# Kernel tuning notes

Hardware: AMD Instinct MI355X
Metric: run time of the kernel (lower is better)

The kernel has to match this reference:

```python
import jax, jax.numpy as jnp
import numpy as np

N, H, C = 65536, 256, 512  # tokens, hidden_dim, cond_dim


def setup_inputs() -> dict:
    key = jax.random.key(0)
    ks = jax.random.split(key, 8)
    s_h = 1.0 / np.sqrt(H)
    s_c = 1.0 / np.sqrt(C)
    return {
        "x": jax.random.normal(ks[0], (N, H), dtype=jnp.float32),
        "cond": jax.random.normal(ks[1], (N, C), dtype=jnp.float32),
        # FiLM: Linear(cond_dim -> 2*hidden_dim), output split into (gamma, beta)
        "W_film": jax.random.uniform(ks[2], (C, 2 * H), jnp.float32, -s_c, s_c),
        "b_film": jax.random.uniform(ks[3], (2 * H,), jnp.float32, -s_c, s_c),
        "W1": jax.random.uniform(ks[4], (H, H), jnp.float32, -s_h, s_h),
        "b1": jax.random.uniform(ks[5], (H,), jnp.float32, -s_h, s_h),
        "W2": jax.random.uniform(ks[6], (H, H), jnp.float32, -s_h, s_h),
        "b2": jax.random.uniform(ks[7], (H,), jnp.float32, -s_h, s_h),
    }


def reference(x, cond, W_film, b_film, W1, b1, W2, b2):
    # FiLM conditioning: gamma * x + beta (cond path; LayerNorm branch unused)
    gb = cond @ W_film + b_film            # [N, 2H]
    gamma, beta = gb[:, :H], gb[:, H:]
    h = gamma * x + beta
    # Dropout is identity in eval mode.
    h = jax.nn.relu(h) @ W1 + b1           # [N, H]
    h = jax.nn.relu(h) @ W2 + b2           # [N, H]
    return h + x                            # residual
```

## Files before the change

### kernel.cpp

```cpp
#include <hip/hip_runtime.h>
#include <hip/hip_bf16.h>


typedef __attribute__((ext_vector_type(8))) short bf16x8;
typedef __attribute__((ext_vector_type(4))) float f32x4;

typedef unsigned short ushort_t;
typedef unsigned int uint_t;

__device__ __forceinline__ ushort_t f2bfh(float f) {
  __hip_bfloat16 h = __float2bfloat16(f);
  return *reinterpret_cast<ushort_t*>(&h);
}
__device__ __forceinline__ float bf2f(ushort_t s) {
  union { uint_t u; float f; } v; v.u = ((uint_t)s) << 16;
  return v.f;
}
__device__ __forceinline__ bf16x8 ldfrag(const ushort_t* p) {
  return *reinterpret_cast<const bf16x8*>(p);
}
__device__ __forceinline__ bf16x8 pack8(float4 a, float4 b) {
  union { bf16x8 v; __hip_bfloat162 h[4]; } u;
  u.h[0] = __float22bfloat162_rn(float2{a.x, a.y});
  u.h[1] = __float22bfloat162_rn(float2{a.z, a.w});
  u.h[2] = __float22bfloat162_rn(float2{b.x, b.y});
  u.h[3] = __float22bfloat162_rn(float2{b.z, b.w});
  return u.v;
}

__global__ void pack_weights(const float* __restrict__ Wf,
                             const float* __restrict__ W1,
                             const float* __restrict__ W2,
                             ushort_t* __restrict__ p1,
                             ushort_t* __restrict__ pW1,
                             ushort_t* __restrict__ pW2) {
  int u = blockIdx.x * 256 + threadIdx.x;
  if (u < 32768) {
    int lane = u & 63, rest = u >> 6;
    int kt = rest & 15;
    int kb = kt * 32 + (lane >> 4) * 8;
    int col = (rest >> 4) * 16 + (lane & 15);
#pragma unroll
    for (int j = 0; j < 8; ++j)
      p1[(size_t)u * 8 + j] = f2bfh(Wf[(size_t)(kb + j) * 512 + col]);
  } else if (u < 40960) {
    int v = u - 32768;
    int lane = v & 63;
    int kt = (v >> 6) & 7;
    int kb = kt * 32 + (lane >> 4) * 8;
    int col = (v >> 9) * 16 + (lane & 15);
#pragma unroll
    for (int j = 0; j < 8; ++j)
      pW1[(size_t)v * 8 + j] = f2bfh(W1[(size_t)(kb + j) * 256 + col]);
  } else if (u < 49152) {
    int v = u - 40960;
    int lane = v & 63;
    int kt = (v >> 6) & 7;
    int kb = kt * 32 + (lane >> 4) * 8;
    int col = (v >> 9) * 16 + (lane & 15);
#pragma unroll
    for (int j = 0; j < 8; ++j)
      pW2[(size_t)v * 8 + j] = f2bfh(W2[(size_t)(kb + j) * 256 + col]);
  }
}

__global__ __launch_bounds__(512, 2)
void film_fused(const float* __restrict__ x, const float* __restrict__ cond,
                const float* __restrict__ b_film, const float* __restrict__ b1,
                const float* __restrict__ b2,
                const ushort_t* __restrict__ p1, const ushort_t* __restrict__ pW1,
                const ushort_t* __restrict__ pW2, float* __restrict__ out) {
  __shared__ __align__(16) char lds[65536];
  const int r0 = blockIdx.x * 64;
  const int t = threadIdx.x;
  const int w = t >> 6;
  const int l = t & 63;
  const int l15 = l & 15;
  const int lhi = l >> 4;

  float bfv[4], b1v[2], b2v[2];
#pragma unroll
  for (int tt = 0; tt < 4; ++tt) bfv[tt] = b_film[w * 64 + tt * 16 + l15];
#pragma unroll
  for (int tt = 0; tt < 2; ++tt) {
    int col = w * 32 + tt * 16 + l15;
    b1v[tt] = b1[col];
    b2v[tt] = b2[col];
  }

#pragma unroll
  for (int it = 0; it < 8; ++it) {
    int u = it * 512 + t;
    int row = u >> 6, k8 = u & 63;
    const float4* cs = reinterpret_cast<const float4*>(cond + (size_t)(r0 + row) * 512 + k8 * 8);
    float4 a = cs[0], b = cs[1];
    int byte = row * 1024 + k8 * 16;
    byte ^= ((row & 15) << 4);
    *reinterpret_cast<bf16x8*>(lds + byte) = pack8(a, b);
  }
  bf16x8 bb[2][4];
#pragma unroll
  for (int tt = 0; tt < 4; ++tt)
    bb[0][tt] = ldfrag(p1 + ((size_t)((w * 4 + tt) * 16 + 0) * 64 + l) * 8);
  __syncthreads();

  f32x4 acc[4][4];
#pragma unroll
  for (int m = 0; m < 4; ++m)
#pragma unroll
    for (int n = 0; n < 4; ++n) acc[m][n] = (f32x4){0.f, 0.f, 0.f, 0.f};

#pragma unroll
  for (int kt = 0; kt < 16; ++kt) {
    const int cur = kt & 1;
    if (kt < 15) {
#pragma unroll
      for (int tt = 0; tt < 4; ++tt)
        bb[cur ^ 1][tt] = ldfrag(p1 + ((size_t)((w * 4 + tt) * 16 + kt + 1) * 64 + l) * 8);
    }
    bf16x8 afr[4];
#pragma unroll
    for (int m = 0; m < 4; ++m) {
      int row = m * 16 + l15;
      int byte = row * 1024 + kt * 64 + lhi * 16;
      byte ^= ((row & 15) << 4);
      afr[m] = *reinterpret_cast<const bf16x8*>(lds + byte);
    }
    __builtin_amdgcn_s_setprio(1);
#pragma unroll
    for (int tt = 0; tt < 4; ++tt)
#pragma unroll
      for (int m = 0; m < 4; ++m)
        acc[m][tt] = __builtin_amdgcn_mfma_f32_16x16x32_bf16(afr[m], bb[cur][tt], acc[m][tt], 0, 0, 0);
    __builtin_amdgcn_s_setprio(0);
  }
  __syncthreads();

#pragma unroll
  for (int tt = 0; tt < 4; ++tt) {
    int col = w * 64 + tt * 16 + l15;
#pragma unroll
    for (int m = 0; m < 4; ++m) {
#pragma unroll
      for (int reg = 0; reg < 4; ++reg) {
        int row = m * 16 + lhi * 4 + reg;
        int byte = row * 1024 + col * 2;
        byte ^= ((row & 15) << 4);
        *reinterpret_cast<ushort_t*>(lds + byte) = f2bfh(acc[m][tt][reg] + bfv[tt]);
      }
    }
  }
  bf16x8 bb2[2][2];
#pragma unroll
  for (int tt = 0; tt < 2; ++tt)
    bb2[0][tt] = ldfrag(pW1 + ((size_t)((w * 2 + tt) * 8 + 0) * 64 + l) * 8);
  __syncthreads();

#pragma unroll
  for (int i = 0; i < 4; ++i) {
    int u = i * 512 + t;
    int row = u >> 5, c8 = u & 31;
    int gbyte = row * 1024 + c8 * 16;
    gbyte ^= ((row & 15) << 4);
    int bbyte = row * 1024 + 512 + c8 * 16;
    bbyte ^= ((row & 15) << 4);
    union { bf16x8 v; ushort_t s[8]; } g, be, r;
    g.v = *reinterpret_cast<const bf16x8*>(lds + gbyte);
    be.v = *reinterpret_cast<const bf16x8*>(lds + bbyte);
    const float4* xs = reinterpret_cast<const float4*>(x + (size_t)(r0 + row) * 256 + c8 * 8);
    float4 xa = xs[0], xb = xs[1];
    float xv[8] = {xa.x, xa.y, xa.z, xa.w, xb.x, xb.y, xb.z, xb.w};
#pragma unroll
    for (int j = 0; j < 8; ++j)
      r.s[j] = f2bfh(fmaxf(bf2f(g.s[j]) * xv[j] + bf2f(be.s[j]), 0.f));
    *reinterpret_cast<bf16x8*>(lds + gbyte) = r.v;
  }
  __syncthreads();

  f32x4 acc2[4][2];
#pragma unroll
  for (int m = 0; m < 4; ++m)
#pragma unroll
    for (int n = 0; n < 2; ++n) acc2[m][n] = (f32x4){0.f, 0.f, 0.f, 0.f};

#pragma unroll
  for (int kt = 0; kt < 8; ++kt) {
    const int cur = kt & 1;
    if (kt < 7) {
#pragma unroll
      for (int tt = 0; tt < 2; ++tt)
        bb2[cur ^ 1][tt] = ldfrag(pW1 + ((size_t)((w * 2 + tt) * 8 + kt + 1) * 64 + l) * 8);
    }
    bf16x8 afr[4];
#pragma unroll
    for (int m = 0; m < 4; ++m) {
      int row = m * 16 + l15;
      int byte = row * 1024 + kt * 64 + lhi * 16;
      byte ^= ((row & 15) << 4);
      afr[m] = *reinterpret_cast<const bf16x8*>(lds + byte);
    }
    __builtin_amdgcn_s_setprio(1);
#pragma unroll
    for (int tt = 0; tt < 2; ++tt)
#pragma unroll
      for (int m = 0; m < 4; ++m)
        acc2[m][tt] = __builtin_amdgcn_mfma_f32_16x16x32_bf16(afr[m], bb2[cur][tt], acc2[m][tt], 0, 0, 0);
    __builtin_amdgcn_s_setprio(0);
  }

  bf16x8 bb3[2][2];
#pragma unroll
  for (int tt = 0; tt < 2; ++tt)
    bb3[0][tt] = ldfrag(pW2 + ((size_t)((w * 2 + tt) * 8 + 0) * 64 + l) * 8);
#pragma unroll
  for (int tt = 0; tt < 2; ++tt) {
    int col = w * 32 + tt * 16 + l15;
#pragma unroll
    for (int m = 0; m < 4; ++m) {
#pragma unroll
      for (int reg = 0; reg < 4; ++reg) {
        int row = m * 16 + lhi * 4 + reg;
        int byte = row * 1024 + 512 + col * 2;
        byte ^= ((row & 15) << 4);
        *reinterpret_cast<ushort_t*>(lds + byte) = f2bfh(fmaxf(acc2[m][tt][reg] + b1v[tt], 0.f));
      }
    }
  }
  __syncthreads();

  f32x4 acc3[4][2];
#pragma unroll
  for (int m = 0; m < 4; ++m)
#pragma unroll
    for (int n = 0; n < 2; ++n) acc3[m][n] = (f32x4){0.f, 0.f, 0.f, 0.f};

#pragma unroll
  for (int kt = 0; kt < 8; ++kt) {
    const int cur = kt & 1;
    if (kt < 7) {
#pragma unroll
      for (int tt = 0; tt < 2; ++tt)
        bb3[cur ^ 1][tt] = ldfrag(pW2 + ((size_t)((w * 2 + tt) * 8 + kt + 1) * 64 + l) * 8);
    }
    bf16x8 afr[4];
#pragma unroll
    for (int m = 0; m < 4; ++m) {
      int row = m * 16 + l15;
      int byte = row * 1024 + 512 + kt * 64 + lhi * 16;
      byte ^= ((row & 15) << 4);
      afr[m] = *reinterpret_cast<const bf16x8*>(lds + byte);
    }
    __builtin_amdgcn_s_setprio(1);
#pragma unroll
    for (int tt = 0; tt < 2; ++tt)
#pragma unroll
      for (int m = 0; m < 4; ++m)
        acc3[m][tt] = __builtin_amdgcn_mfma_f32_16x16x32_bf16(afr[m], bb3[cur][tt], acc3[m][tt], 0, 0, 0);
    __builtin_amdgcn_s_setprio(0);
  }
  __syncthreads();

#pragma unroll
  for (int hh = 0; hh < 2; ++hh) {
    if (hh) __syncthreads();
#pragma unroll
    for (int tt = 0; tt < 2; ++tt) {
      int col = w * 32 + tt * 16 + l15;
#pragma unroll
      for (int mm = 0; mm < 2; ++mm) {
        int m = hh * 2 + mm;
#pragma unroll
        for (int reg = 0; reg < 4; ++reg) {
          int r = mm * 16 + lhi * 4 + reg;
          int byte = r * 1024 + col * 4;
          byte ^= ((r & 15) << 4);
          *reinterpret_cast<float*>(lds + byte) = acc3[m][tt][reg] + b2v[tt];
        }
      }
    }
    __syncthreads();
#pragma unroll
    for (int i = 0; i < 4; ++i) {
      int u = i * 512 + t;
      int r = u >> 6, c4 = u & 63;
      int byte = r * 1024 + c4 * 16;
      byte ^= ((r & 15) << 4);
      f32x4 v = *reinterpret_cast<const f32x4*>(lds + byte);
      int grow = hh * 32 + r;
      const float4 xres = *reinterpret_cast<const float4*>(
          x + (size_t)(r0 + grow) * 256 + c4 * 4);
      v.x += xres.x; v.y += xres.y; v.z += xres.z; v.w += xres.w;
      f32x4* op = reinterpret_cast<f32x4*>(out + (size_t)(r0 + grow) * 256 + c4 * 4);
      __builtin_nontemporal_store(v, op);
    }
  }
}

extern "C" void kernel_launch(void* const* d_in, const int* in_sizes, int n_in,
                              void* d_out, int out_size, void* d_ws, size_t ws_size,
                              hipStream_t stream) {
  const float* x      = (const float*)d_in[0];
  const float* cond   = (const float*)d_in[1];
  const float* W_film = (const float*)d_in[2];
  const float* b_film = (const float*)d_in[3];
  const float* W1     = (const float*)d_in[4];
  const float* b1     = (const float*)d_in[5];
  const float* W2     = (const float*)d_in[6];
  const float* b2     = (const float*)d_in[7];
  float* out = (float*)d_out;

  ushort_t* p1  = (ushort_t*)d_ws;
  ushort_t* pW1 = p1 + 262144;
  ushort_t* pW2 = pW1 + 65536;

  hipLaunchKernelGGL(pack_weights, dim3(192), dim3(256), 0, stream,
                     W_film, W1, W2, p1, pW1, pW2);
  hipLaunchKernelGGL(film_fused, dim3(1024), dim3(512), 0, stream,
                     x, cond, b_film, b1, b2, p1, pW1, pW2, out);
}
```

Baseline: 99.48 us.

## Stream cond tiles into an LDS ring via async global_load_lds

The upfront cond load now bypasses registers. Each 64-column fp32 chunk is fetched asynchronously with global_load_lds into a four-slot LDS ring and prefetched two chunks ahead of the FiLM GEMM. Fragments are read back as fp32 from the XOR-swizzled slots and packed to bf16 just before the MFMA. The aim is to overlap the cond fetch with matrix work instead of stalling on one large staging phase. The cost is double the LDS read traffic, bf16 conversion inside the MFMA loop, and a barrier every chunk, which may also force full vmcnt waits.

```diff
diff --git a/kernel.cpp b/kernel.cpp
--- a/kernel.cpp
+++ b/kernel.cpp
@@ -25,6 +25,14 @@
   u.h[1] = __float22bfloat162_rn(float2{a.z, a.w});
   u.h[2] = __float22bfloat162_rn(float2{b.x, b.y});
   u.h[3] = __float22bfloat162_rn(float2{b.z, b.w});
+  return u.v;
+}
+__device__ __forceinline__ bf16x8 pack8v(f32x4 a, f32x4 b) {
+  union { bf16x8 v; __hip_bfloat162 h[4]; } u;
+  u.h[0] = __float22bfloat162_rn(float2{a[0], a[1]});
+  u.h[1] = __float22bfloat162_rn(float2{a[2], a[3]});
+  u.h[2] = __float22bfloat162_rn(float2{b[0], b[1]});
+  u.h[3] = __float22bfloat162_rn(float2{b[2], b[3]});
   return u.v;
 }
 
@@ -88,16 +96,24 @@
     b2v[tt] = b2[col];
   }
 
-#pragma unroll
-  for (int it = 0; it < 8; ++it) {
-    int u = it * 512 + t;
-    int row = u >> 6, k8 = u & 63;
-    const float4* cs = reinterpret_cast<const float4*>(cond + (size_t)(r0 + row) * 512 + k8 * 8);
-    float4 a = cs[0], b = cs[1];
-    int byte = row * 1024 + k8 * 16;
-    byte ^= ((row & 15) << 4);
-    *reinterpret_cast<bf16x8*>(lds + byte) = pack8(a, b);
-  }
+  const char* condb = reinterpret_cast<const char*>(cond);
+#define STAGE_CHUNK(c)                                                        \
+  {                                                                           \
+    char* qb = lds + ((c) & 3) * 16384;                                       \
+    _Pragma("unroll")                                                         \
+    for (int i = 0; i < 2; ++i) {                                             \
+      int u = i * 512 + t;                                                    \
+      int row = u >> 4, slot = u & 15;                                        \
+      const char* g = condb + (size_t)(r0 + row) * 2048 + (c) * 256 +         \
+                      ((slot ^ (row & 15)) << 4);                             \
+      __builtin_amdgcn_global_load_lds(                                       \
+          (const __attribute__((address_space(1))) void*)g,                   \
+          (__attribute__((address_space(3))) void*)(qb + u * 16), 16, 0, 0);  \
+    }                                                                         \
+  }
+
+  STAGE_CHUNK(0)
+  STAGE_CHUNK(1)
   bf16x8 bb[2][4];
 #pragma unroll
   for (int tt = 0; tt < 4; ++tt)
@@ -111,30 +127,38 @@
     for (int n = 0; n < 4; ++n) acc[m][n] = (f32x4){0.f, 0.f, 0.f, 0.f};
 
 #pragma unroll
-  for (int kt = 0; kt < 16; ++kt) {
-    const int cur = kt & 1;
-    if (kt < 15) {
+  for (int c = 0; c < 8; ++c) {
+    if (c < 6) STAGE_CHUNK(c + 2)
+    const char* qb = lds + (c & 3) * 16384;
+#pragma unroll
+    for (int ktl = 0; ktl < 2; ++ktl) {
+      const int kt = c * 2 + ktl;
+      const int cur = kt & 1;
+      if (kt < 15) {
+#pragma unroll
+        for (int tt = 0; tt < 4; ++tt)
+          bb[cur ^ 1][tt] = ldfrag(p1 + ((size_t)((w * 4 + tt) * 16 + kt + 1) * 64 + l) * 8);
+      }
+      bf16x8 afr[4];
+#pragma unroll
+      for (int m = 0; m < 4; ++m) {
+        int row = m * 16 + l15;
+        int sw = row & 15;
+        int s0 = ktl * 8 + lhi * 2;
+        f32x4 f0 = *reinterpret_cast<const f32x4*>(qb + row * 256 + ((s0 ^ sw) << 4));
+        f32x4 f1 = *reinterpret_cast<const f32x4*>(qb + row * 256 + (((s0 + 1) ^ sw) << 4));
+        afr[m] = pack8v(f0, f1);
+      }
+      __builtin_amdgcn_s_setprio(1);
 #pragma unroll
       for (int tt = 0; tt < 4; ++tt)
-        bb[cur ^ 1][tt] = ldfrag(p1 + ((size_t)((w * 4 + tt) * 16 + kt + 1) * 64 + l) * 8);
-    }
-    bf16x8 afr[4];
-#pragma unroll
-    for (int m = 0; m < 4; ++m) {
-      int row = m * 16 + l15;
-      int byte = row * 1024 + kt * 64 + lhi * 16;
-      byte ^= ((row & 15) << 4);
-      afr[m] = *reinterpret_cast<const bf16x8*>(lds + byte);
-    }
-    __builtin_amdgcn_s_setprio(1);
-#pragma unroll
-    for (int tt = 0; tt < 4; ++tt)
-#pragma unroll
-      for (int m = 0; m < 4; ++m)
-        acc[m][tt] = __builtin_amdgcn_mfma_f32_16x16x32_bf16(afr[m], bb[cur][tt], acc[m][tt], 0, 0, 0);
-    __builtin_amdgcn_s_setprio(0);
-  }
-  __syncthreads();
+#pragma unroll
+        for (int m = 0; m < 4; ++m)
+          acc[m][tt] = __builtin_amdgcn_mfma_f32_16x16x32_bf16(afr[m], bb[cur][tt], acc[m][tt], 0, 0, 0);
+      __builtin_amdgcn_s_setprio(0);
+    }
+    __syncthreads();
+  }
 
 #pragma unroll
   for (int tt = 0; tt < 4; ++tt) {
@@ -294,6 +318,7 @@
       __builtin_nontemporal_store(v, op);
     }
   }
+#undef STAGE_CHUNK
 }
 
 extern "C" void kernel_launch(void* const* d_in, const int* in_sizes, int n_in,
```

After: 97.54 us. About the same (-1.9%).

## Shrink row tile to 32 with 16 waves per block and fuse FiLM epilogue

Applied to the files above, without the earlier changes.

Each block now handles 32 rows with 1024 threads, so each wave owns one 16-column slice of gamma and beta plus a 16-column slice of the hidden outputs. LDS drops to 32 KB and per-wave accumulators shrink, which raises the launch bound to 4 blocks per CU. The FiLM multiply-add is applied directly from the gamma and beta accumulators against x staged in LDS, so the bf16 gb round trip through LDS is gone. The cost is less register reuse of weight fragments per row and more global weight fragment loads per output row, plus non-unrolled K loops. x is also rounded to bf16 before the FiLM multiply, which adds a small precision loss.

```diff
diff --git a/kernel.cpp b/kernel.cpp
--- a/kernel.cpp
+++ b/kernel.cpp
@@ -64,33 +64,30 @@
   }
 }
 
-__global__ __launch_bounds__(512, 2)
+__global__ __launch_bounds__(1024, 4)
 void film_fused(const float* __restrict__ x, const float* __restrict__ cond,
                 const float* __restrict__ b_film, const float* __restrict__ b1,
                 const float* __restrict__ b2,
                 const ushort_t* __restrict__ p1, const ushort_t* __restrict__ pW1,
                 const ushort_t* __restrict__ pW2, float* __restrict__ out) {
-  __shared__ __align__(16) char lds[65536];
-  const int r0 = blockIdx.x * 64;
+  __shared__ __align__(16) char lds[32768];
+  char* A = lds;
+  char* B = lds + 16384;
+  const int r0 = blockIdx.x * 32;
   const int t = threadIdx.x;
   const int w = t >> 6;
   const int l = t & 63;
   const int l15 = l & 15;
   const int lhi = l >> 4;
 
-  float bfv[4], b1v[2], b2v[2];
-#pragma unroll
-  for (int tt = 0; tt < 4; ++tt) bfv[tt] = b_film[w * 64 + tt * 16 + l15];
-#pragma unroll
-  for (int tt = 0; tt < 2; ++tt) {
-    int col = w * 32 + tt * 16 + l15;
-    b1v[tt] = b1[col];
-    b2v[tt] = b2[col];
-  }
-
-#pragma unroll
-  for (int it = 0; it < 8; ++it) {
-    int u = it * 512 + t;
+  const float bgv = b_film[w * 16 + l15];
+  const float bbv = b_film[256 + w * 16 + l15];
+  const float b1v = b1[w * 16 + l15];
+  const float b2v = b2[w * 16 + l15];
+
+#pragma unroll
+  for (int it = 0; it < 2; ++it) {
+    int u = it * 1024 + t;
     int row = u >> 6, k8 = u & 63;
     const float4* cs = reinterpret_cast<const float4*>(cond + (size_t)(r0 + row) * 512 + k8 * 8);
     float4 a = cs[0], b = cs[1];
@@ -98,201 +95,177 @@
     byte ^= ((row & 15) << 4);
     *reinterpret_cast<bf16x8*>(lds + byte) = pack8(a, b);
   }
-  bf16x8 bb[2][4];
-#pragma unroll
-  for (int tt = 0; tt < 4; ++tt)
-    bb[0][tt] = ldfrag(p1 + ((size_t)((w * 4 + tt) * 16 + 0) * 64 + l) * 8);
-  __syncthreads();
-
-  f32x4 acc[4][4];
-#pragma unroll
-  for (int m = 0; m < 4; ++m)
-#pragma unroll
-    for (int n = 0; n < 4; ++n) acc[m][n] = (f32x4){0.f, 0.f, 0.f, 0.f};
-
-#pragma unroll
-  for (int kt = 0; kt < 16; ++kt) {
-    const int cur = kt & 1;
-    if (kt < 15) {
-#pragma unroll
-      for (int tt = 0; tt < 4; ++tt)
-        bb[cur ^ 1][tt] = ldfrag(p1 + ((size_t)((w * 4 + tt) * 16 + kt + 1) * 64 + l) * 8);
-    }
-    bf16x8 afr[4];
-#pragma unroll
-    for (int m = 0; m < 4; ++m) {
-      int row = m * 16 + l15;
-      int byte = row * 1024 + kt * 64 + lhi * 16;
-      byte ^= ((row & 15) << 4);
-      afr[m] = *reinterpret_cast<const bf16x8*>(lds + byte);
-    }
-    __builtin_amdgcn_s_setprio(1);
-#pragma unroll
-    for (int tt = 0; tt < 4; ++tt)
-#pragma unroll
-      for (int m = 0; m < 4; ++m)
-        acc[m][tt] = __builtin_amdgcn_mfma_f32_16x16x32_bf16(afr[m], bb[cur][tt], acc[m][tt], 0, 0, 0);
-    __builtin_amdgcn_s_setprio(0);
-  }
-  __syncthreads();
-
-#pragma unroll
-  for (int tt = 0; tt < 4; ++tt) {
-    int col = w * 64 + tt * 16 + l15;
-#pragma unroll
-    for (int m = 0; m < 4; ++m) {
-#pragma unroll
-      for (int reg = 0; reg < 4; ++reg) {
-        int row = m * 16 + lhi * 4 + reg;
-        int byte = row * 1024 + col * 2;
-        byte ^= ((row & 15) << 4);
-        *reinterpret_cast<ushort_t*>(lds + byte) = f2bfh(acc[m][tt][reg] + bfv[tt]);
-      }
-    }
-  }
-  bf16x8 bb2[2][2];
-#pragma unroll
-  for (int tt = 0; tt < 2; ++tt)
-    bb2[0][tt] = ldfrag(pW1 + ((size_t)((w * 2 + tt) * 8 + 0) * 64 + l) * 8);
-  __syncthreads();
-
-#pragma unroll
-  for (int i = 0; i < 4; ++i) {
-    int u = i * 512 + t;
-    int row = u >> 5, c8 = u & 31;
-    int gbyte = row * 1024 + c8 * 16;
-    gbyte ^= ((row & 15) << 4);
-    int bbyte = row * 1024 + 512 + c8 * 16;
-    bbyte ^= ((row & 15) << 4);
-    union { bf16x8 v; ushort_t s[8]; } g, be, r;
-    g.v = *reinterpret_cast<const bf16x8*>(lds + gbyte);
-    be.v = *reinterpret_cast<const bf16x8*>(lds + bbyte);
+  bf16x8 bcg = ldfrag(p1 + ((size_t)(w * 16 + 0) * 64 + l) * 8);
+  bf16x8 bcb = ldfrag(p1 + ((size_t)((16 + w) * 16 + 0) * 64 + l) * 8);
+  __syncthreads();
+
+  f32x4 accg[2], accb[2];
+#pragma unroll
+  for (int m = 0; m < 2; ++m) {
+    accg[m] = (f32x4){0.f, 0.f, 0.f, 0.f};
+    accb[m] = (f32x4){0.f, 0.f, 0.f, 0.f};
+  }
+
+#pragma unroll 1
+  for (int kp = 0; kp < 8; ++kp) {
+    const int kt0 = kp * 2;
+    bf16x8 bng = ldfrag(p1 + ((size_t)(w * 16 + kt0 + 1) * 64 + l) * 8);
+    bf16x8 bnb = ldfrag(p1 + ((size_t)((16 + w) * 16 + kt0 + 1) * 64 + l) * 8);
+    __builtin_amdgcn_s_setprio(1);
+#pragma unroll
+    for (int m = 0; m < 2; ++m) {
+      int row = m * 16 + l15;
+      int byte = row * 1024 + kt0 * 64 + lhi * 16;
+      byte ^= ((row & 15) << 4);
+      bf16x8 a = *reinterpret_cast<const bf16x8*>(lds + byte);
+      accg[m] = __builtin_amdgcn_mfma_f32_16x16x32_bf16(a, bcg, accg[m], 0, 0, 0);
+      accb[m] = __builtin_amdgcn_mfma_f32_16x16x32_bf16(a, bcb, accb[m], 0, 0, 0);
+    }
+    __builtin_amdgcn_s_setprio(0);
+    if (kt0 + 2 < 16) {
+      bcg = ldfrag(p1 + ((size_t)(w * 16 + kt0 + 2) * 64 + l) * 8);
+      bcb = ldfrag(p1 + ((size_t)((16 + w) * 16 + kt0 + 2) * 64 + l) * 8);
+    }
+    __builtin_amdgcn_s_setprio(1);
+#pragma unroll
+    for (int m = 0; m < 2; ++m) {
+      int row = m * 16 + l15;
+      int byte = row * 1024 + (kt0 + 1) * 64 + lhi * 16;
+      byte ^= ((row & 15) << 4);
+      bf16x8 a = *reinterpret_cast<const bf16x8*>(lds + byte);
+      accg[m] = __builtin_amdgcn_mfma_f32_16x16x32_bf16(a, bng, accg[m], 0, 0, 0);
+      accb[m] = __builtin_amdgcn_mfma_f32_16x16x32_bf16(a, bnb, accb[m], 0, 0, 0);
+    }
+    __builtin_amdgcn_s_setprio(0);
+  }
+  __syncthreads();
+
+  {
+    int row = t >> 5, c8 = t & 31;
     const float4* xs = reinterpret_cast<const float4*>(x + (size_t)(r0 + row) * 256 + c8 * 8);
     float4 xa = xs[0], xb = xs[1];
-    float xv[8] = {xa.x, xa.y, xa.z, xa.w, xb.x, xb.y, xb.z, xb.w};
-#pragma unroll
-    for (int j = 0; j < 8; ++j)
-      r.s[j] = f2bfh(fmaxf(bf2f(g.s[j]) * xv[j] + bf2f(be.s[j]), 0.f));
-    *reinterpret_cast<bf16x8*>(lds + gbyte) = r.v;
-  }
-  __syncthreads();
-
-  f32x4 acc2[4][2];
-#pragma unroll
-  for (int m = 0; m < 4; ++m)
-#pragma unroll
-    for (int n = 0; n < 2; ++n) acc2[m][n] = (f32x4){0.f, 0.f, 0.f, 0.f};
-
-#pragma unroll
-  for (int kt = 0; kt < 8; ++kt) {
-    const int cur = kt & 1;
-    if (kt < 7) {
-#pragma unroll
-      for (int tt = 0; tt < 2; ++tt)
-        bb2[cur ^ 1][tt] = ldfrag(pW1 + ((size_t)((w * 2 + tt) * 8 + kt + 1) * 64 + l) * 8);
-    }
-    bf16x8 afr[4];
-#pragma unroll
-    for (int m = 0; m < 4; ++m) {
-      int row = m * 16 + l15;
-      int byte = row * 1024 + kt * 64 + lhi * 16;
-      byte ^= ((row & 15) << 4);
-      afr[m] = *reinterpret_cast<const bf16x8*>(lds + byte);
-    }
-    __builtin_amdgcn_s_setprio(1);
-#pragma unroll
-    for (int tt = 0; tt < 2; ++tt)
-#pragma unroll
-      for (int m = 0; m < 4; ++m)
-        acc2[m][tt] = __builtin_amdgcn_mfma_f32_16x16x32_bf16(afr[m], bb2[cur][tt], acc2[m][tt], 0, 0, 0);
-    __builtin_amdgcn_s_setprio(0);
-  }
-
-  bf16x8 bb3[2][2];
-#pragma unroll
-  for (int tt = 0; tt < 2; ++tt)
-    bb3[0][tt] = ldfrag(pW2 + ((size_t)((w * 2 + tt) * 8 + 0) * 64 + l) * 8);
-#pragma unroll
-  for (int tt = 0; tt < 2; ++tt) {
-    int col = w * 32 + tt * 16 + l15;
-#pragma unroll
-    for (int m = 0; m < 4; ++m) {
-#pragma unroll
-      for (int reg = 0; reg < 4; ++reg) {
-        int row = m * 16 + lhi * 4 + reg;
-        int byte = row * 1024 + 512 + col * 2;
-        byte ^= ((row & 15) << 4);
-        *reinterpret_cast<ushort_t*>(lds + byte) = f2bfh(fmaxf(acc2[m][tt][reg] + b1v[tt], 0.f));
-      }
-    }
-  }
-  __syncthreads();
-
-  f32x4 acc3[4][2];
-#pragma unroll
-  for (int m = 0; m < 4; ++m)
-#pragma unroll
-    for (int n = 0; n < 2; ++n) acc3[m][n] = (f32x4){0.f, 0.f, 0.f, 0.f};
-
-#pragma unroll
-  for (int kt = 0; kt < 8; ++kt) {
-    const int cur = kt & 1;
-    if (kt < 7) {
-#pragma unroll
-      for (int tt = 0; tt < 2; ++tt)
-        bb3[cur ^ 1][tt] = ldfrag(pW2 + ((size_t)((w * 2 + tt) * 8 + kt + 1) * 64 + l) * 8);
-    }
-    bf16x8 afr[4];
-#pragma unroll
-    for (int m = 0; m < 4; ++m) {
-      int row = m * 16 + l15;
-      int byte = row * 1024 + 512 + kt * 64 + lhi * 16;
-      byte ^= ((row & 15) << 4);
-      afr[m] = *reinterpret_cast<const bf16x8*>(lds + byte);
-    }
-    __builtin_amdgcn_s_setprio(1);
-#pragma unroll
-    for (int tt = 0; tt < 2; ++tt)
-#pragma unroll
-      for (int m = 0; m < 4; ++m)
-        acc3[m][tt] = __builtin_amdgcn_mfma_f32_16x16x32_bf16(afr[m], bb3[cur][tt], acc3[m][tt], 0, 0, 0);
-    __builtin_amdgcn_s_setprio(0);
-  }
-  __syncthreads();
-
-#pragma unroll
-  for (int hh = 0; hh < 2; ++hh) {
-    if (hh) __syncthreads();
-#pragma unroll
-    for (int tt = 0; tt < 2; ++tt) {
-      int col = w * 32 + tt * 16 + l15;
-#pragma unroll
-      for (int mm = 0; mm < 2; ++mm) {
-        int m = hh * 2 + mm;
-#pragma unroll
-        for (int reg = 0; reg < 4; ++reg) {
-          int r = mm * 16 + lhi * 4 + reg;
-          int byte = r * 1024 + col * 4;
-          byte ^= ((r & 15) << 4);
-          *reinterpret_cast<float*>(lds + byte) = acc3[m][tt][reg] + b2v[tt];
-        }
-      }
-    }
-    __syncthreads();
-#pragma unroll
-    for (int i = 0; i < 4; ++i) {
-      int u = i * 512 + t;
-      int r = u >> 6, c4 = u & 63;
-      int byte = r * 1024 + c4 * 16;
-      byte ^= ((r & 15) << 4);
-      f32x4 v = *reinterpret_cast<const f32x4*>(lds + byte);
-      int grow = hh * 32 + r;
-      const float4 xres = *reinterpret_cast<const float4*>(
-          x + (size_t)(r0 + grow) * 256 + c4 * 4);
-      v.x += xres.x; v.y += xres.y; v.z += xres.z; v.w += xres.w;
-      f32x4* op = reinterpret_cast<f32x4*>(out + (size_t)(r0 + grow) * 256 + c4 * 4);
-      __builtin_nontemporal_store(v, op);
-    }
+    int byte = row * 512 + c8 * 16;
+    byte ^= ((row & 15) << 4);
+    *reinterpret_cast<bf16x8*>(A + byte) = pack8(xa, xb);
+  }
+  __syncthreads();
+
+#pragma unroll
+  for (int m = 0; m < 2; ++m) {
+#pragma unroll
+    for (int reg = 0; reg < 4; ++reg) {
+      int row = m * 16 + lhi * 4 + reg;
+      int col = w * 16 + l15;
+      int byte = row * 512 + col * 2;
+      byte ^= ((row & 15) << 4);
+      float xv = bf2f(*reinterpret_cast<const ushort_t*>(A + byte));
+      float hv = fmaxf((accg[m][reg] + bgv) * xv + (accb[m][reg] + bbv), 0.f);
+      *reinterpret_cast<ushort_t*>(B + byte) = f2bfh(hv);
+    }
+  }
+  bf16x8 c2 = ldfrag(pW1 + ((size_t)(w * 8 + 0) * 64 + l) * 8);
+  __syncthreads();
+
+  f32x4 acc2[2];
+#pragma unroll
+  for (int m = 0; m < 2; ++m) acc2[m] = (f32x4){0.f, 0.f, 0.f, 0.f};
+
+#pragma unroll 1
+  for (int kp = 0; kp < 4; ++kp) {
+    const int kt0 = kp * 2;
+    bf16x8 n2 = ldfrag(pW1 + ((size_t)(w * 8 + kt0 + 1) * 64 + l) * 8);
+    __builtin_amdgcn_s_setprio(1);
+#pragma unroll
+    for (int m = 0; m < 2; ++m) {
+      int row = m * 16 + l15;
+      int byte = row * 512 + kt0 * 64 + lhi * 16;
+      byte ^= ((row & 15) << 4);
+      bf16x8 a = *reinterpret_cast<const bf16x8*>(B + byte);
+      acc2[m] = __builtin_amdgcn_mfma_f32_16x16x32_bf16(a, c2, acc2[m], 0, 0, 0);
+    }
+    __builtin_amdgcn_s_setprio(0);
+    if (kt0 + 2 < 8) c2 = ldfrag(pW1 + ((size_t)(w * 8 + kt0 + 2) * 64 + l) * 8);
+    __builtin_amdgcn_s_setprio(1);
+#pragma unroll
+    for (int m = 0; m < 2; ++m) {
+      int row = m * 16 + l15;
+      int byte = row * 512 + (kt0 + 1) * 64 + lhi * 16;
+      byte ^= ((row & 15) << 4);
+      bf16x8 a = *reinterpret_cast<const bf16x8*>(B + byte);
+      acc2[m] = __builtin_amdgcn_mfma_f32_16x16x32_bf16(a, n2, acc2[m], 0, 0, 0);
+    }
+    __builtin_amdgcn_s_setprio(0);
+  }
+#pragma unroll
+  for (int m = 0; m < 2; ++m) {
+#pragma unroll
+    for (int reg = 0; reg < 4; ++reg) {
+      int row = m * 16 + lhi * 4 + reg;
+      int col = w * 16 + l15;
+      int byte = row * 512 + col * 2;
+      byte ^= ((row & 15) << 4);
+      *reinterpret_cast<ushort_t*>(A + byte) = f2bfh(fmaxf(acc2[m][reg] + b1v, 0.f));
+    }
+  }
+  bf16x8 c3 = ldfrag(pW2 + ((size_t)(w * 8 + 0) * 64 + l) * 8);
+  __syncthreads();
+
+  f32x4 acc3[2];
+#pragma unroll
+  for (int m = 0; m < 2; ++m) acc3[m] = (f32x4){0.f, 0.f, 0.f, 0.f};
+
+#pragma unroll 1
+  for (int kp = 0; kp < 4; ++kp) {
+    const int kt0 = kp * 2;
+    bf16x8 n3 = ldfrag(pW2 + ((size_t)(w * 8 + kt0 + 1) * 64 + l) * 8);
+    __builtin_amdgcn_s_setprio(1);
+#pragma unroll
+    for (int m = 0; m < 2; ++m) {
+      int row = m * 16 + l15;
+      int byte = row * 512 + kt0 * 64 + lhi * 16;
+      byte ^= ((row & 15) << 4);
+      bf16x8 a = *reinterpret_cast<const bf16x8*>(A + byte);
+      acc3[m] = __builtin_amdgcn_mfma_f32_16x16x32_bf16(a, c3, acc3[m], 0, 0, 0);
+    }
+    __builtin_amdgcn_s_setprio(0);
+    if (kt0 + 2 < 8) c3 = ldfrag(pW2 + ((size_t)(w * 8 + kt0 + 2) * 64 + l) * 8);
+    __builtin_amdgcn_s_setprio(1);
+#pragma unroll
+    for (int m = 0; m < 2; ++m) {
+      int row = m * 16 + l15;
+      int byte = row * 512 + (kt0 + 1) * 64 + lhi * 16;
+      byte ^= ((row & 15) << 4);
+      bf16x8 a = *reinterpret_cast<const bf16x8*>(A + byte);
+      acc3[m] = __builtin_amdgcn_mfma_f32_16x16x32_bf16(a, n3, acc3[m], 0, 0, 0);
+    }
+    __builtin_amdgcn_s_setprio(0);
+  }
+  __syncthreads();
+
+#pragma unroll
+  for (int m = 0; m < 2; ++m) {
+#pragma unroll
+    for (int reg = 0; reg < 4; ++reg) {
+      int row = m * 16 + lhi * 4 + reg;
+      int col = w * 16 + l15;
+      int byte = row * 1024 + col * 4;
+      byte ^= ((row & 15) << 4);
+      *reinterpret_cast<float*>(lds + byte) = acc3[m][reg] + b2v;
+    }
+  }
+  __syncthreads();
+#pragma unroll
+  for (int i = 0; i < 2; ++i) {
+    int u = i * 1024 + t;
+    int row = u >> 6, c4 = u & 63;
+    int byte = row * 1024 + c4 * 16;
+    byte ^= ((row & 15) << 4);
+    f32x4 v = *reinterpret_cast<const f32x4*>(lds + byte);
+    const float4 xres = *reinterpret_cast<const float4*>(
+        x + (size_t)(r0 + row) * 256 + c4 * 4);
+    v.x += xres.x; v.y += xres.y; v.z += xres.z; v.w += xres.w;
+    f32x4* op = reinterpret_cast<f32x4*>(out + (size_t)(r0 + row) * 256 + c4 * 4);
+    __builtin_nontemporal_store(v, op);
   }
 }
 
@@ -315,6 +288,6 @@
 
   hipLaunchKernelGGL(pack_weights, dim3(192), dim3(256), 0, stream,
                      W_film, W1, W2, p1, pW1, pW2);
-  hipLaunchKernelGGL(film_fused, dim3(1024), dim3(512), 0, stream,
+  hipLaunchKernelGGL(film_fused, dim3(2048), dim3(1024), 0, stream,
                      x, cond, b_film, b1, b2, p1, pW1, pW2, out);
 }
```

Result: slower. 113.4 us (+14.0%).
